# Optimization experiments

Measured on AMD Instinct MI355X. Metric: run time of the kernel, lower is better.

Reference implementation:

```python
import jax, jax.numpy as jnp
import numpy as np

TABLE_SIZE = 2 ** 18  # log2_hashmap_size = 18
N_LEVELS = 8
PRIME_Y = np.uint32(2654435761)
PRIME_Z = np.uint32(805459861)
# 8 cube-corner offsets in {0,1}^3
CORNERS = jnp.asarray([[(c >> d) & 1 for d in range(3)] for c in range(8)], dtype=jnp.int32)  # [8,3]


def setup_inputs() -> dict:
    key = jax.random.key(0)
    ks = jax.random.split(key, 6)
    N = 2_097_152
    x = jax.random.uniform(ks[0], (N, 3), dtype=jnp.float32)          # points in [0,1]^3
    mesh_min = jnp.zeros((3,), jnp.float32)
    mesh_max = jnp.ones((3,), jnp.float32)
    # tcnn initializes grid features uniform in [-1e-4, 1e-4]
    tables = jax.random.uniform(ks[1], (N_LEVELS, TABLE_SIZE, 2), jnp.float32, -1e-4, 1e-4)
    w_in = jax.random.normal(ks[2], (16, 64), jnp.float32) * (1.0 / np.sqrt(16))
    w_hidden = jax.random.normal(ks[3], (3, 64, 64), jnp.float32) * (1.0 / np.sqrt(64))
    w_out = jax.random.normal(ks[4], (64, 1), jnp.float32) * (1.0 / np.sqrt(64))
    return {"x": x, "mesh_min": mesh_min, "mesh_max": mesh_max,
            "tables": tables, "w_in": w_in, "w_hidden": w_hidden, "w_out": w_out}


def _hashgrid_encode(u, tables):
    """u: [N,3] in [0,1]. tables: [L, T, F]. Returns [N, L*F]."""
    feats = []
    for l in range(N_LEVELS):
        res = 2 * (2 ** l)  # base_resolution=2, per_level_scale=2
        pos = u * res                                   # [N,3]
        c0 = jnp.floor(pos).astype(jnp.int32)
        w = pos - c0                                    # trilinear fractions, [N,3]
        corners = jnp.clip(c0[:, None, :] + CORNERS[None], 0, res)  # [N,8,3]
        if (res + 1) ** 3 <= TABLE_SIZE:
            # dense grid: no hashing needed at coarse levels
            idx = (corners[..., 0]
                   + corners[..., 1] * (res + 1)
                   + corners[..., 2] * (res + 1) ** 2)
        else:
            uc = corners.astype(jnp.uint32)
            h = uc[..., 0] ^ (uc[..., 1] * PRIME_Y) ^ (uc[..., 2] * PRIME_Z)
            idx = (h % jnp.uint32(TABLE_SIZE)).astype(jnp.int32)
        # trilinear weights per corner: prod over dims of w or (1-w)
        wt = jnp.prod(jnp.where(CORNERS[None] == 1, w[:, None, :], 1.0 - w[:, None, :]), axis=-1)  # [N,8]
        feats.append(jnp.einsum('nc,ncf->nf', wt, tables[l][idx]))  # [N,F]
    return jnp.concatenate(feats, axis=-1)  # [N, L*F] = [N,16]


def reference(x, mesh_min, mesh_max, tables, w_in, w_hidden, w_out):
    u = (x - mesh_min) / (mesh_max - mesh_min)          # normalize to [0,1]^3
    enc = _hashgrid_encode(u, tables)                   # [N,16]
    h = jax.nn.relu(enc @ w_in)                         # [N,64]
    for i in range(w_hidden.shape[0]):                  # 3 more hidden layers (4 total)
        h = jax.nn.relu(h @ w_hidden[i])
    out = (h @ w_out).squeeze(-1)                       # [N], no output activation
    return out
```

## Files before the change

### kernel.cpp

```cpp
#include <hip/hip_runtime.h>
#include <stdint.h>

typedef _Float16 half2v __attribute__((ext_vector_type(2)));
typedef _Float16 half4 __attribute__((ext_vector_type(4)));
typedef _Float16 half8 __attribute__((ext_vector_type(8)));
typedef float floatx4 __attribute__((ext_vector_type(4)));
typedef float float4u __attribute__((ext_vector_type(4), aligned(8)));

#define TPB 256
#define ENC_ROW 20

__device__ __forceinline__ half2v pkrtz(float a, float b) {
    return __builtin_bit_cast(half2v, __builtin_amdgcn_cvt_pkrtz(a, b));
}

__device__ __forceinline__ half4 relu_pack(floatx4 c) {
    half2v lo = pkrtz(fmaxf(c[0], 0.f), fmaxf(c[1], 0.f));
    half2v hi = pkrtz(fmaxf(c[2], 0.f), fmaxf(c[3], 0.f));
    half4 r;
    r[0] = lo[0]; r[1] = lo[1]; r[2] = hi[0]; r[3] = hi[1];
    return r;
}

__global__ void prep_weights(const float* __restrict__ w_in,
                             const float* __restrict__ w_hidden,
                             _Float16* __restrict__ ws) {
    int i = blockIdx.x * 256 + threadIdx.x;
    if (i < 1024) {
        int j = i & 3, lane = (i >> 2) & 63, mt = i >> 8;
        int k = ((lane >> 4) & 3) * 4 + j;
        int n = mt * 16 + (lane & 15);
        ws[i] = (_Float16)w_in[k * 64 + n];
    } else if (i < 13312) {
        int t = i - 1024;
        int j = t & 3, lane = (t >> 2) & 63;
        int mt = (t >> 8) & 3, kt = (t >> 10) & 3, layer = t >> 12;
        int k = kt * 16 + ((lane >> 4) & 3) * 4 + j;
        int n = mt * 16 + (lane & 15);
        ws[i] = (_Float16)w_hidden[layer * 4096 + k * 64 + n];
    }
}

__global__ void prep_tables(const float* __restrict__ tables,
                            uint32_t* __restrict__ tf) {
    int i = blockIdx.x * 256 + threadIdx.x;
    float2 v = ((const float2*)tables)[i];
    half2v h;
    h[0] = (_Float16)(v.x * 8192.f);
    h[1] = (_Float16)(v.y * 8192.f);
    tf[i] = __builtin_bit_cast(uint32_t, h);
}

__global__ __launch_bounds__(TPB, 4) void encode_kernel(
    const float* __restrict__ x,
    const float* __restrict__ mesh_min,
    const float* __restrict__ mesh_max,
    const float* __restrict__ tables,
    const uint32_t* __restrict__ tabs,
    _Float16* __restrict__ enc,
    int N) {
    __shared__ float2 ltab[881];

    const int p = blockIdx.x * TPB + threadIdx.x;

    {
        const float2* t0 = (const float2*)tables;
        for (int i = threadIdx.x; i < 27; i += TPB) ltab[i] = t0[i];
        const float2* t1 = (const float2*)(tables + 1 * 524288);
        for (int i = threadIdx.x; i < 125; i += TPB) ltab[27 + i] = t1[i];
        const float2* t2 = (const float2*)(tables + 2 * 524288);
        for (int i = threadIdx.x; i < 729; i += TPB) ltab[152 + i] = t2[i];
    }
    __syncthreads();

    float mn0 = mesh_min[0], mn1 = mesh_min[1], mn2 = mesh_min[2];
    float mx0 = mesh_max[0], mx1 = mesh_max[1], mx2 = mesh_max[2];
    float ux = (x[3 * p + 0] - mn0) / (mx0 - mn0);
    float uy = (x[3 * p + 1] - mn1) / (mx1 - mn1);
    float uz = (x[3 * p + 2] - mn2) / (mx2 - mn2);

    float ef[16];
    float wl[3][3];
    uint32_t g[24];

#pragma unroll
    for (int l = 0; l < 3; ++l) {
        const int res = 64 << l;
        const uint32_t* tab = tabs + (size_t)(l + 5) * 262144;
        float px = ux * (float)res, py = uy * (float)res, pz = uz * (float)res;
        int cx = (int)floorf(px), cy = (int)floorf(py), cz = (int)floorf(pz);
        wl[l][0] = px - (float)cx;
        wl[l][1] = py - (float)cy;
        wl[l][2] = pz - (float)cz;
        uint32_t hy0 = (uint32_t)cy * 2654435761u, hy1 = (uint32_t)(cy + 1) * 2654435761u;
        uint32_t hz0 = (uint32_t)cz * 805459861u,  hz1 = (uint32_t)(cz + 1) * 805459861u;
#pragma unroll
        for (int c = 0; c < 4; ++c) {
            uint32_t hyz = ((c & 1) ? hy1 : hy0) ^ ((c & 2) ? hz1 : hz0);
            uint32_t i0 = ((uint32_t)cx ^ hyz) & 262143u;
            uint32_t i1 = ((uint32_t)(cx + 1) ^ hyz) & 262143u;
            g[l * 8 + 2 * c + 0] = tab[i0];
            g[l * 8 + 2 * c + 1] = tab[i1];
        }
    }

#pragma unroll
    for (int l = 3; l < 5; ++l) {
        const int res = 2 << l;
        const int s = res + 1;
        const uint32_t* tab = tabs + (size_t)l * 262144;
        float px = ux * (float)res, py = uy * (float)res, pz = uz * (float)res;
        int cx = (int)floorf(px), cy = (int)floorf(py), cz = (int)floorf(pz);
        float wx = px - (float)cx, wy = py - (float)cy, wz = pz - (float)cz;
        float f0 = 0.f, f1 = 0.f;
#pragma unroll
        for (int c = 0; c < 4; ++c) {
            int Y = cy + ((c & 1) ? 1 : 0);
            int Z = cz + ((c & 2) ? 1 : 0);
            float wyz = ((c & 1) ? wy : 1.f - wy) * ((c & 2) ? wz : 1.f - wz);
            int i0 = cx + Y * s + Z * s * s;
            uint32_t v0 = tab[i0];
            uint32_t v1 = tab[i0 + 1];
            half2v e0 = __builtin_bit_cast(half2v, v0);
            half2v e1 = __builtin_bit_cast(half2v, v1);
            f0 += wyz * ((float)e0[0] + wx * ((float)e1[0] - (float)e0[0]));
            f1 += wyz * ((float)e0[1] + wx * ((float)e1[1] - (float)e0[1]));
        }
        ef[2 * l + 0] = f0;
        ef[2 * l + 1] = f1;
    }

#pragma unroll
    for (int l = 0; l < 3; ++l) {
        const int res = 2 << l;
        const int s = res + 1;
        const int base = (l == 0) ? 0 : (l == 1) ? 27 : 152;
        float px = ux * (float)res, py = uy * (float)res, pz = uz * (float)res;
        int cx = (int)floorf(px), cy = (int)floorf(py), cz = (int)floorf(pz);
        float wx = px - (float)cx, wy = py - (float)cy, wz = pz - (float)cz;
        float f0 = 0.f, f1 = 0.f;
#pragma unroll
        for (int c = 0; c < 4; ++c) {
            int i0 = base + cx + (cy + ((c & 1) ? 1 : 0)) * s + (cz + ((c & 2) ? 1 : 0)) * s * s;
            float wyz = ((c & 1) ? wy : 1.f - wy) * ((c & 2) ? wz : 1.f - wz);
            float2 e0 = ltab[i0];
            float2 e1 = ltab[i0 + 1];
            f0 += wyz * (e0.x + wx * (e1.x - e0.x));
            f1 += wyz * (e0.y + wx * (e1.y - e0.y));
        }
        ef[2 * l + 0] = f0 * 8192.f;
        ef[2 * l + 1] = f1 * 8192.f;
    }

#pragma unroll
    for (int l = 0; l < 3; ++l) {
        float wx = wl[l][0], wy = wl[l][1], wz = wl[l][2];
        float f0 = 0.f, f1 = 0.f;
#pragma unroll
        for (int c = 0; c < 4; ++c) {
            float wyz = ((c & 1) ? wy : 1.f - wy) * ((c & 2) ? wz : 1.f - wz);
            half2v e0 = __builtin_bit_cast(half2v, g[l * 8 + 2 * c + 0]);
            half2v e1 = __builtin_bit_cast(half2v, g[l * 8 + 2 * c + 1]);
            f0 += wyz * ((float)e0[0] + wx * ((float)e1[0] - (float)e0[0]));
            f1 += wyz * ((float)e0[1] + wx * ((float)e1[1] - (float)e0[1]));
        }
        ef[10 + 2 * l + 0] = f0;
        ef[10 + 2 * l + 1] = f1;
    }

    half8 lo, hi;
#pragma unroll
    for (int v = 0; v < 4; ++v) {
        half2v a = pkrtz(ef[4 * v + 0], ef[4 * v + 1]);
        half2v b = pkrtz(ef[4 * v + 2], ef[4 * v + 3]);
        if (v < 2) { lo[4*v+0]=a[0]; lo[4*v+1]=a[1]; lo[4*v+2]=b[0]; lo[4*v+3]=b[1]; }
        else       { int w = v-2; hi[4*w+0]=a[0]; hi[4*w+1]=a[1]; hi[4*w+2]=b[0]; hi[4*w+3]=b[1]; }
    }
    *(half8*)(enc + ((size_t)p << 4) + 0) = lo;
    *(half8*)(enc + ((size_t)p << 4) + 8) = hi;
}

__global__ __launch_bounds__(TPB, 4) void mlp_kernel(
    const _Float16* __restrict__ enc,
    const _Float16* __restrict__ ws,
    const float* __restrict__ w_out,
    float* __restrict__ out,
    int N) {
    const int wave = threadIdx.x >> 6;
    const int lane = threadIdx.x & 63;
    const int l15 = lane & 15;
    const int quad = lane >> 4;
    const int wavebase = blockIdx.x * TPB + wave * 64;

    floatx4 C[4][4];

    {
        half4 b[4];
#pragma unroll
        for (int nt = 0; nt < 4; ++nt)
            b[nt] = *(const half4*)(enc + ((size_t)(wavebase + nt * 16 + l15) << 4) + quad * 4);
#pragma unroll
        for (int mt = 0; mt < 4; ++mt) {
            half4 a = *(const half4*)(ws + mt * 256 + lane * 4);
#pragma unroll
            for (int nt = 0; nt < 4; ++nt) {
                floatx4 zero = {0.f, 0.f, 0.f, 0.f};
                C[mt][nt] = __builtin_amdgcn_mfma_f32_16x16x16f16(a, b[nt], zero, 0, 0, 0);
            }
        }
    }

#pragma unroll
    for (int layer = 0; layer < 3; ++layer) {
        half4 b[4][4];
#pragma unroll
        for (int kt = 0; kt < 4; ++kt)
#pragma unroll
            for (int nt = 0; nt < 4; ++nt)
                b[kt][nt] = relu_pack(C[kt][nt]);
#pragma unroll
        for (int mt = 0; mt < 4; ++mt) {
            half4 a[4];
#pragma unroll
            for (int kt = 0; kt < 4; ++kt)
                a[kt] = *(const half4*)(ws + 1024 + ((layer * 4 + kt) * 4 + mt) * 256 + lane * 4);
#pragma unroll
            for (int nt = 0; nt < 4; ++nt) {
                floatx4 acc = {0.f, 0.f, 0.f, 0.f};
#pragma unroll
                for (int kt = 0; kt < 4; ++kt)
                    acc = __builtin_amdgcn_mfma_f32_16x16x16f16(a[kt], b[kt][nt], acc, 0, 0, 0);
                C[mt][nt] = acc;
            }
        }
    }

    {
        float s[4] = {0.f, 0.f, 0.f, 0.f};
#pragma unroll
        for (int mt = 0; mt < 4; ++mt) {
            float4 wo = *(const float4*)(w_out + mt * 16 + quad * 4);
#pragma unroll
            for (int nt = 0; nt < 4; ++nt) {
                s[nt] = fmaf(fmaxf(C[mt][nt][0], 0.f), wo.x, s[nt]);
                s[nt] = fmaf(fmaxf(C[mt][nt][1], 0.f), wo.y, s[nt]);
                s[nt] = fmaf(fmaxf(C[mt][nt][2], 0.f), wo.z, s[nt]);
                s[nt] = fmaf(fmaxf(C[mt][nt][3], 0.f), wo.w, s[nt]);
            }
        }
#pragma unroll
        for (int nt = 0; nt < 4; ++nt) {
            s[nt] += __shfl_xor(s[nt], 16, 64);
            s[nt] += __shfl_xor(s[nt], 32, 64);
        }
        float r = (quad & 1) ? ((quad & 2) ? s[3] : s[1])
                             : ((quad & 2) ? s[2] : s[0]);
        out[wavebase + quad * 16 + l15] = r * (1.f / 8192.f);
    }
}

__global__ __launch_bounds__(TPB, 4) void hashgrid_mlp_kernel(
    const float* __restrict__ x,
    const float* __restrict__ mesh_min,
    const float* __restrict__ mesh_max,
    const float* __restrict__ tables,
    const _Float16* __restrict__ ws,
    const float* __restrict__ w_out,
    float* __restrict__ out,
    int N) {
    __shared__ float2 ltab[881];
    __shared__ _Float16 encbuf[4][64][ENC_ROW];

    const int wave = threadIdx.x >> 6;
    const int lane = threadIdx.x & 63;
    const int l15 = lane & 15;
    const int quad = lane >> 4;
    const int wavebase = blockIdx.x * TPB + wave * 64;
    const int p = wavebase + lane;

    {
        const float2* t0 = (const float2*)tables;
        for (int i = threadIdx.x; i < 27; i += TPB) ltab[i] = t0[i];
        const float2* t1 = (const float2*)(tables + 1 * 524288);
        for (int i = threadIdx.x; i < 125; i += TPB) ltab[27 + i] = t1[i];
        const float2* t2 = (const float2*)(tables + 2 * 524288);
        for (int i = threadIdx.x; i < 729; i += TPB) ltab[152 + i] = t2[i];
    }

    float mn0 = mesh_min[0], mn1 = mesh_min[1], mn2 = mesh_min[2];
    float mx0 = mesh_max[0], mx1 = mesh_max[1], mx2 = mesh_max[2];
    float ux = (x[3 * p + 0] - mn0) / (mx0 - mn0);
    float uy = (x[3 * p + 1] - mn1) / (mx1 - mn1);
    float uz = (x[3 * p + 2] - mn2) / (mx2 - mn2);

    float ef[16];
    float wl[3][3];
    float2 g[24];

#pragma unroll
    for (int l = 0; l < 3; ++l) {
        const int res = 64 << l;
        const float* tab = tables + (size_t)(l + 5) * 524288;
        float px = ux * (float)res, py = uy * (float)res, pz = uz * (float)res;
        int cx = (int)floorf(px), cy = (int)floorf(py), cz = (int)floorf(pz);
        wl[l][0] = px - (float)cx;
        wl[l][1] = py - (float)cy;
        wl[l][2] = pz - (float)cz;
        uint32_t hy0 = (uint32_t)cy * 2654435761u, hy1 = (uint32_t)(cy + 1) * 2654435761u;
        uint32_t hz0 = (uint32_t)cz * 805459861u,  hz1 = (uint32_t)(cz + 1) * 805459861u;
#pragma unroll
        for (int c = 0; c < 4; ++c) {
            uint32_t hyz = ((c & 1) ? hy1 : hy0) ^ ((c & 2) ? hz1 : hz0);
            uint32_t i0 = ((uint32_t)cx ^ hyz) & 262143u;
            uint32_t i1 = ((uint32_t)(cx + 1) ^ hyz) & 262143u;
            g[l * 8 + 2 * c + 0] = *(const float2*)(tab + 2 * (size_t)i0);
            g[l * 8 + 2 * c + 1] = *(const float2*)(tab + 2 * (size_t)i1);
        }
    }

#pragma unroll
    for (int l = 3; l < 5; ++l) {
        const int res = 2 << l;
        const int s = res + 1;
        const float* tab = tables + (size_t)l * 524288;
        float px = ux * (float)res, py = uy * (float)res, pz = uz * (float)res;
        int cx = (int)floorf(px), cy = (int)floorf(py), cz = (int)floorf(pz);
        float wx = px - (float)cx, wy = py - (float)cy, wz = pz - (float)cz;
        float f0 = 0.f, f1 = 0.f;
#pragma unroll
        for (int c = 0; c < 4; ++c) {
            int Y = cy + ((c & 1) ? 1 : 0);
            int Z = cz + ((c & 2) ? 1 : 0);
            float wyz = ((c & 1) ? wy : 1.f - wy) * ((c & 2) ? wz : 1.f - wz);
            int i0 = cx + Y * s + Z * s * s;
            float4u v = *(const float4u*)(tab + 2 * (size_t)i0);
            f0 += wyz * (v.x + wx * (v.z - v.x));
            f1 += wyz * (v.y + wx * (v.w - v.y));
        }
        ef[2 * l + 0] = f0;
        ef[2 * l + 1] = f1;
    }

    __syncthreads();

#pragma unroll
    for (int l = 0; l < 3; ++l) {
        const int res = 2 << l;
        const int s = res + 1;
        const int base = (l == 0) ? 0 : (l == 1) ? 27 : 152;
        float px = ux * (float)res, py = uy * (float)res, pz = uz * (float)res;
        int cx = (int)floorf(px), cy = (int)floorf(py), cz = (int)floorf(pz);
        float wx = px - (float)cx, wy = py - (float)cy, wz = pz - (float)cz;
        float f0 = 0.f, f1 = 0.f;
#pragma unroll
        for (int c = 0; c < 4; ++c) {
            int i0 = base + cx + (cy + ((c & 1) ? 1 : 0)) * s + (cz + ((c & 2) ? 1 : 0)) * s * s;
            float wyz = ((c & 1) ? wy : 1.f - wy) * ((c & 2) ? wz : 1.f - wz);
            float2 e0 = ltab[i0];
            float2 e1 = ltab[i0 + 1];
            f0 += wyz * (e0.x + wx * (e1.x - e0.x));
            f1 += wyz * (e0.y + wx * (e1.y - e0.y));
        }
        ef[2 * l + 0] = f0;
        ef[2 * l + 1] = f1;
    }

#pragma unroll
    for (int l = 0; l < 3; ++l) {
        float wx = wl[l][0], wy = wl[l][1], wz = wl[l][2];
        float f0 = 0.f, f1 = 0.f;
#pragma unroll
        for (int c = 0; c < 4; ++c) {
            float wyz = ((c & 1) ? wy : 1.f - wy) * ((c & 2) ? wz : 1.f - wz);
            float2 e0 = g[l * 8 + 2 * c + 0];
            float2 e1 = g[l * 8 + 2 * c + 1];
            f0 += wyz * (e0.x + wx * (e1.x - e0.x));
            f1 += wyz * (e0.y + wx * (e1.y - e0.y));
        }
        ef[10 + 2 * l + 0] = f0;
        ef[10 + 2 * l + 1] = f1;
    }

#pragma unroll
    for (int v = 0; v < 4; ++v) {
        half2v lo = pkrtz(ef[4 * v + 0] * 8192.f, ef[4 * v + 1] * 8192.f);
        half2v hi = pkrtz(ef[4 * v + 2] * 8192.f, ef[4 * v + 3] * 8192.f);
        half4 t;
        t[0] = lo[0]; t[1] = lo[1]; t[2] = hi[0]; t[3] = hi[1];
        *(half4*)&encbuf[wave][lane][v * 4] = t;
    }

    floatx4 C[4][4];
    {
        half4 b[4];
#pragma unroll
        for (int nt = 0; nt < 4; ++nt)
            b[nt] = *(const half4*)&encbuf[wave][nt * 16 + l15][quad * 4];
#pragma unroll
        for (int mt = 0; mt < 4; ++mt) {
            half4 a = *(const half4*)(ws + mt * 256 + lane * 4);
#pragma unroll
            for (int nt = 0; nt < 4; ++nt) {
                floatx4 zero = {0.f, 0.f, 0.f, 0.f};
                C[mt][nt] = __builtin_amdgcn_mfma_f32_16x16x16f16(a, b[nt], zero, 0, 0, 0);
            }
        }
    }

#pragma unroll
    for (int layer = 0; layer < 3; ++layer) {
        half4 b[4][4];
#pragma unroll
        for (int kt = 0; kt < 4; ++kt)
#pragma unroll
            for (int nt = 0; nt < 4; ++nt)
                b[kt][nt] = relu_pack(C[kt][nt]);
#pragma unroll
        for (int mt = 0; mt < 4; ++mt) {
            half4 a[4];
#pragma unroll
            for (int kt = 0; kt < 4; ++kt)
                a[kt] = *(const half4*)(ws + 1024 + ((layer * 4 + kt) * 4 + mt) * 256 + lane * 4);
#pragma unroll
            for (int nt = 0; nt < 4; ++nt) {
                floatx4 acc = {0.f, 0.f, 0.f, 0.f};
#pragma unroll
                for (int kt = 0; kt < 4; ++kt)
                    acc = __builtin_amdgcn_mfma_f32_16x16x16f16(a[kt], b[kt][nt], acc, 0, 0, 0);
                C[mt][nt] = acc;
            }
        }
    }

    {
        float s[4] = {0.f, 0.f, 0.f, 0.f};
#pragma unroll
        for (int mt = 0; mt < 4; ++mt) {
            float4 wo = *(const float4*)(w_out + mt * 16 + quad * 4);
#pragma unroll
            for (int nt = 0; nt < 4; ++nt) {
                s[nt] = fmaf(fmaxf(C[mt][nt][0], 0.f), wo.x, s[nt]);
                s[nt] = fmaf(fmaxf(C[mt][nt][1], 0.f), wo.y, s[nt]);
                s[nt] = fmaf(fmaxf(C[mt][nt][2], 0.f), wo.z, s[nt]);
                s[nt] = fmaf(fmaxf(C[mt][nt][3], 0.f), wo.w, s[nt]);
            }
        }
#pragma unroll
        for (int nt = 0; nt < 4; ++nt) {
            s[nt] += __shfl_xor(s[nt], 16, 64);
            s[nt] += __shfl_xor(s[nt], 32, 64);
        }
        float r = (quad & 1) ? ((quad & 2) ? s[3] : s[1])
                             : ((quad & 2) ? s[2] : s[0]);
        out[wavebase + quad * 16 + l15] = r * (1.f / 8192.f);
    }
}

extern "C" void kernel_launch(void* const* d_in, const int* in_sizes, int n_in,
                              void* d_out, int out_size, void* d_ws,
                              size_t ws_size, hipStream_t stream) {
    const float* x        = (const float*)d_in[0];
    const float* mesh_min = (const float*)d_in[1];
    const float* mesh_max = (const float*)d_in[2];
    const float* tables   = (const float*)d_in[3];
    const float* w_in     = (const float*)d_in[4];
    const float* w_hidden = (const float*)d_in[5];
    const float* w_out    = (const float*)d_in[6];
    float* out = (float*)d_out;
    _Float16* ws = (_Float16*)d_ws;

    int N = out_size;

    hipLaunchKernelGGL(prep_weights, dim3(52), dim3(256), 0, stream,
                       w_in, w_hidden, ws);

    size_t enc_off  = 32768 / 2;
    size_t tab_off  = enc_off + (size_t)N * 16;
    size_t need     = 32768 + (size_t)N * 32 + (size_t)8 * 262144 * 4;
    if (ws_size >= need) {
        _Float16* enc = ws + enc_off;
        uint32_t* tf  = (uint32_t*)(ws + tab_off);
        hipLaunchKernelGGL(prep_tables, dim3(8192), dim3(256), 0, stream,
                           tables, tf);
        hipLaunchKernelGGL(encode_kernel, dim3(N / TPB), dim3(TPB), 0, stream,
                           x, mesh_min, mesh_max, tables, tf, enc, N);
        hipLaunchKernelGGL(mlp_kernel, dim3(N / TPB), dim3(TPB), 0, stream,
                           enc, ws, w_out, out, N);
    } else {
        hipLaunchKernelGGL(hashgrid_mlp_kernel, dim3(N / TPB), dim3(TPB), 0, stream,
                           x, mesh_min, mesh_max, tables, ws, w_out, out, N);
    }
}
```

Measured before the change: 304.1 us.

## Fuse hashgrid encode and MLP into one kernel with LDS staging

Merges the encode and MLP kernels so the 16-wide fp16 encoding passes through a per-wave LDS buffer instead of a global round trip of N*32 bytes. Level 3's dense table (4913 entries) now also sits in shared memory. Level-4 gathers are issued early and consumed after the barrier to overlap latency. The cost is extra LDS per block (about 37KB total), which may reduce occupancy below the launch-bounds target, and a block-wide sync that now guards more data.

```diff
diff --git a/kernel.cpp b/kernel.cpp
--- a/kernel.cpp
+++ b/kernel.cpp
@@ -51,17 +51,26 @@
     tf[i] = __builtin_bit_cast(uint32_t, h);
 }
 
-__global__ __launch_bounds__(TPB, 4) void encode_kernel(
+__global__ __launch_bounds__(TPB, 4) void fused_kernel(
     const float* __restrict__ x,
     const float* __restrict__ mesh_min,
     const float* __restrict__ mesh_max,
     const float* __restrict__ tables,
     const uint32_t* __restrict__ tabs,
-    _Float16* __restrict__ enc,
+    const _Float16* __restrict__ ws,
+    const float* __restrict__ w_out,
+    float* __restrict__ out,
     int N) {
     __shared__ float2 ltab[881];
-
-    const int p = blockIdx.x * TPB + threadIdx.x;
+    __shared__ uint32_t l3tab[4913];
+    __shared__ _Float16 encbuf[4][64][ENC_ROW];
+
+    const int wave = threadIdx.x >> 6;
+    const int lane = threadIdx.x & 63;
+    const int l15 = lane & 15;
+    const int quad = lane >> 4;
+    const int wavebase = blockIdx.x * TPB + wave * 64;
+    const int p = wavebase + lane;
 
     {
         const float2* t0 = (const float2*)tables;
@@ -70,8 +79,9 @@
         for (int i = threadIdx.x; i < 125; i += TPB) ltab[27 + i] = t1[i];
         const float2* t2 = (const float2*)(tables + 2 * 524288);
         for (int i = threadIdx.x; i < 729; i += TPB) ltab[152 + i] = t2[i];
-    }
-    __syncthreads();
+        const uint32_t* t3 = tabs + 3 * 262144;
+        for (int i = threadIdx.x; i < 4913; i += TPB) l3tab[i] = t3[i];
+    }
 
     float mn0 = mesh_min[0], mn1 = mesh_min[1], mn2 = mesh_min[2];
     float mx0 = mesh_max[0], mx1 = mesh_max[1], mx2 = mesh_max[2];
@@ -82,6 +92,8 @@
     float ef[16];
     float wl[3][3];
     uint32_t g[24];
+    uint32_t g4[8];
+    float w4x, w4y, w4z;
 
 #pragma unroll
     for (int l = 0; l < 3; ++l) {
@@ -104,31 +116,24 @@
         }
     }
 
-#pragma unroll
-    for (int l = 3; l < 5; ++l) {
-        const int res = 2 << l;
-        const int s = res + 1;
-        const uint32_t* tab = tabs + (size_t)l * 262144;
-        float px = ux * (float)res, py = uy * (float)res, pz = uz * (float)res;
-        int cx = (int)floorf(px), cy = (int)floorf(py), cz = (int)floorf(pz);
-        float wx = px - (float)cx, wy = py - (float)cy, wz = pz - (float)cz;
-        float f0 = 0.f, f1 = 0.f;
+    {
+        const int res = 32, s = 33;
+        const uint32_t* tab = tabs + (size_t)4 * 262144;
+        float px = ux * 32.f, py = uy * 32.f, pz = uz * 32.f;
+        int cx = (int)floorf(px), cy = (int)floorf(py), cz = (int)floorf(pz);
+        w4x = px - (float)cx; w4y = py - (float)cy; w4z = pz - (float)cz;
+        (void)res;
 #pragma unroll
         for (int c = 0; c < 4; ++c) {
             int Y = cy + ((c & 1) ? 1 : 0);
             int Z = cz + ((c & 2) ? 1 : 0);
-            float wyz = ((c & 1) ? wy : 1.f - wy) * ((c & 2) ? wz : 1.f - wz);
             int i0 = cx + Y * s + Z * s * s;
-            uint32_t v0 = tab[i0];
-            uint32_t v1 = tab[i0 + 1];
-            half2v e0 = __builtin_bit_cast(half2v, v0);
-            half2v e1 = __builtin_bit_cast(half2v, v1);
-            f0 += wyz * ((float)e0[0] + wx * ((float)e1[0] - (float)e0[0]));
-            f1 += wyz * ((float)e0[1] + wx * ((float)e1[1] - (float)e0[1]));
-        }
-        ef[2 * l + 0] = f0;
-        ef[2 * l + 1] = f1;
-    }
+            g4[2 * c + 0] = tab[i0];
+            g4[2 * c + 1] = tab[i0 + 1];
+        }
+    }
+
+    __syncthreads();
 
 #pragma unroll
     for (int l = 0; l < 3; ++l) {
@@ -152,6 +157,39 @@
         ef[2 * l + 1] = f1 * 8192.f;
     }
 
+    {
+        const int s = 17;
+        float px = ux * 16.f, py = uy * 16.f, pz = uz * 16.f;
+        int cx = (int)floorf(px), cy = (int)floorf(py), cz = (int)floorf(pz);
+        float wx = px - (float)cx, wy = py - (float)cy, wz = pz - (float)cz;
+        float f0 = 0.f, f1 = 0.f;
+#pragma unroll
+        for (int c = 0; c < 4; ++c) {
+            int i0 = cx + (cy + ((c & 1) ? 1 : 0)) * s + (cz + ((c & 2) ? 1 : 0)) * s * s;
+            float wyz = ((c & 1) ? wy : 1.f - wy) * ((c & 2) ? wz : 1.f - wz);
+            half2v e0 = __builtin_bit_cast(half2v, l3tab[i0]);
+            half2v e1 = __builtin_bit_cast(half2v, l3tab[i0 + 1]);
+            f0 += wyz * ((float)e0[0] + wx * ((float)e1[0] - (float)e0[0]));
+            f1 += wyz * ((float)e0[1] + wx * ((float)e1[1] - (float)e0[1]));
+        }
+        ef[6] = f0;
+        ef[7] = f1;
+    }
+
+    {
+        float f0 = 0.f, f1 = 0.f;
+#pragma unroll
+        for (int c = 0; c < 4; ++c) {
+            float wyz = ((c & 1) ? w4y : 1.f - w4y) * ((c & 2) ? w4z : 1.f - w4z);
+            half2v e0 = __builtin_bit_cast(half2v, g4[2 * c + 0]);
+            half2v e1 = __builtin_bit_cast(half2v, g4[2 * c + 1]);
+            f0 += wyz * ((float)e0[0] + w4x * ((float)e1[0] - (float)e0[0]));
+            f1 += wyz * ((float)e0[1] + w4x * ((float)e1[1] - (float)e0[1]));
+        }
+        ef[8] = f0;
+        ef[9] = f1;
+    }
+
 #pragma unroll
     for (int l = 0; l < 3; ++l) {
         float wx = wl[l][0], wy = wl[l][1], wz = wl[l][2];
@@ -168,37 +206,21 @@
         ef[10 + 2 * l + 1] = f1;
     }
 
-    half8 lo, hi;
 #pragma unroll
     for (int v = 0; v < 4; ++v) {
-        half2v a = pkrtz(ef[4 * v + 0], ef[4 * v + 1]);
-        half2v b = pkrtz(ef[4 * v + 2], ef[4 * v + 3]);
-        if (v < 2) { lo[4*v+0]=a[0]; lo[4*v+1]=a[1]; lo[4*v+2]=b[0]; lo[4*v+3]=b[1]; }
-        else       { int w = v-2; hi[4*w+0]=a[0]; hi[4*w+1]=a[1]; hi[4*w+2]=b[0]; hi[4*w+3]=b[1]; }
-    }
-    *(half8*)(enc + ((size_t)p << 4) + 0) = lo;
-    *(half8*)(enc + ((size_t)p << 4) + 8) = hi;
-}
-
-__global__ __launch_bounds__(TPB, 4) void mlp_kernel(
-    const _Float16* __restrict__ enc,
-    const _Float16* __restrict__ ws,
-    const float* __restrict__ w_out,
-    float* __restrict__ out,
-    int N) {
-    const int wave = threadIdx.x >> 6;
-    const int lane = threadIdx.x & 63;
-    const int l15 = lane & 15;
-    const int quad = lane >> 4;
-    const int wavebase = blockIdx.x * TPB + wave * 64;
+        half2v lo = pkrtz(ef[4 * v + 0], ef[4 * v + 1]);
+        half2v hi = pkrtz(ef[4 * v + 2], ef[4 * v + 3]);
+        half4 t;
+        t[0] = lo[0]; t[1] = lo[1]; t[2] = hi[0]; t[3] = hi[1];
+        *(half4*)&encbuf[wave][lane][v * 4] = t;
+    }
 
     floatx4 C[4][4];
-
     {
         half4 b[4];
 #pragma unroll
         for (int nt = 0; nt < 4; ++nt)
-            b[nt] = *(const half4*)(enc + ((size_t)(wavebase + nt * 16 + l15) << 4) + quad * 4);
+            b[nt] = *(const half4*)&encbuf[wave][nt * 16 + l15][quad * 4];
 #pragma unroll
         for (int mt = 0; mt < 4; ++mt) {
             half4 a = *(const half4*)(ws + mt * 256 + lane * 4);
@@ -474,18 +496,13 @@
     hipLaunchKernelGGL(prep_weights, dim3(52), dim3(256), 0, stream,
                        w_in, w_hidden, ws);
 
-    size_t enc_off  = 32768 / 2;
-    size_t tab_off  = enc_off + (size_t)N * 16;
-    size_t need     = 32768 + (size_t)N * 32 + (size_t)8 * 262144 * 4;
+    size_t need = 32768 + (size_t)8 * 262144 * 4;
     if (ws_size >= need) {
-        _Float16* enc = ws + enc_off;
-        uint32_t* tf  = (uint32_t*)(ws + tab_off);
+        uint32_t* tf = (uint32_t*)((char*)d_ws + 32768);
         hipLaunchKernelGGL(prep_tables, dim3(8192), dim3(256), 0, stream,
                            tables, tf);
-        hipLaunchKernelGGL(encode_kernel, dim3(N / TPB), dim3(TPB), 0, stream,
-                           x, mesh_min, mesh_max, tables, tf, enc, N);
-        hipLaunchKernelGGL(mlp_kernel, dim3(N / TPB), dim3(TPB), 0, stream,
-                           enc, ws, w_out, out, N);
+        hipLaunchKernelGGL(fused_kernel, dim3(N / TPB), dim3(TPB), 0, stream,
+                           x, mesh_min, mesh_max, tables, tf, ws, w_out, out, N);
     } else {
         hipLaunchKernelGGL(hashgrid_mlp_kernel, dim3(N / TPB), dim3(TPB), 0, stream,
                            x, mesh_min, mesh_max, tables, ws, w_out, out, N);
```

After: 269.8 us. -11.3%, faster.
